# Performance work log

Hardware: AMD Instinct MI355X
Metric: run time of the kernel (lower is better)

The kernel has to match this reference:

```python
import jax, jax.numpy as jnp
import numpy as np

EMBED = 1024
HEADS = 16
HEAD_DIM = EMBED // HEADS


def setup_inputs() -> dict:
    key = jax.random.key(0)
    ks = jax.random.split(key, 6)
    N, L = 2, 2048
    s = 1.0 / np.sqrt(EMBED)
    x = jax.random.normal(ks[0], (N, L, EMBED), dtype=jnp.float32)
    Wq = jax.random.normal(ks[1], (EMBED, EMBED), dtype=jnp.float32) * s
    Wk = jax.random.normal(ks[2], (EMBED, EMBED), dtype=jnp.float32) * s
    Wv = jax.random.normal(ks[3], (EMBED, EMBED), dtype=jnp.float32) * s
    Wo = jax.random.normal(ks[4], (EMBED, EMBED), dtype=jnp.float32) * s
    bo = jax.random.normal(ks[5], (EMBED,), dtype=jnp.float32) * 0.01
    return {"x": x, "Wq": Wq, "Wk": Wk, "Wv": Wv, "Wo": Wo, "bo": bo}


def reference(x, Wq, Wk, Wv, Wo, bo):
    N, L, E = x.shape
    # QKV projections (torch Linear: x @ W.T), split into heads: (N, L, H, D)
    q = (x @ Wq.T).reshape(N, L, HEADS, HEAD_DIM)
    k = (x @ Wk.T).reshape(N, L, HEADS, HEAD_DIM)
    v = (x @ Wv.T).reshape(N, L, HEADS, HEAD_DIM)
    # scores: (N, H, Lq, Lk), scaled by 1/sqrt(embed_size) as in the source
    scores = jnp.einsum("nqhd,nkhd->nhqk", q, k) / jnp.sqrt(jnp.float32(E))
    attn = jax.nn.softmax(scores, axis=-1)
    out = jnp.einsum("nhqk,nkhd->nqhd", attn, v).reshape(N, L, E)
    return out @ Wo.T + bo
```

## Files before the change

### kernel.cpp

```cpp
#include <hip/hip_runtime.h>
#include <hip/hip_bf16.h>
#include <stdint.h>


#define SEQ    2048
#define EMBED  1024
#define QS     3072
#define MTOT   4096
#define SOFTMAX_C 0.04508422002778011f

using bf16x8 = __attribute__((ext_vector_type(8))) __bf16;
using bf16x4 = __attribute__((ext_vector_type(4))) __bf16;
using f32x4  = __attribute__((ext_vector_type(4))) float;

__device__ __forceinline__ unsigned short f2bf(float f) {
  unsigned u = __builtin_bit_cast(unsigned, f);
  u += 0x7fffu + ((u >> 16) & 1u);
  return (unsigned short)(u >> 16);
}
__device__ __forceinline__ float bf2f(unsigned short h) {
  return __builtin_bit_cast(float, (unsigned)h << 16);
}

__device__ __forceinline__ void gl_lds16(const void* g, void* l) {
  __builtin_amdgcn_global_load_lds(
      (const __attribute__((address_space(1))) unsigned int*)g,
      (__attribute__((address_space(3))) unsigned int*)l, 16, 0, 0);
}

__global__ void __launch_bounds__(256) convert_all(
    const float* __restrict__ x, const float* __restrict__ Wq,
    const float* __restrict__ Wk, const float* __restrict__ Wv,
    const float* __restrict__ Wo, unsigned short* __restrict__ xbf,
    unsigned short* __restrict__ wqkv, unsigned short* __restrict__ wo) {
  int b = blockIdx.x;
  int c4 = threadIdx.x << 2;
  const float* src;
  unsigned short* dst;
  if (b < 4096) {
    src = x + (size_t)b * EMBED;
    dst = xbf + (size_t)b * 1024;
  } else if (b < 7168) {
    int R = b - 4096;
    const float* W = (R < 1024) ? Wq : (R < 2048) ? Wk : Wv;
    src = W + (size_t)(R & 1023) * EMBED;
    dst = wqkv + (size_t)R * 1024;
  } else {
    int r = b - 7168;
    src = Wo + (size_t)r * EMBED;
    dst = wo + (size_t)r * 1024;
  }
  float4 v = *(const float4*)(src + c4);
  *(ushort4*)(dst + c4) = make_ushort4(f2bf(v.x), f2bf(v.y), f2bf(v.z), f2bf(v.w));
}

template <int MODE>
__global__ void __launch_bounds__(256, 4) gemm_bt(
    const unsigned short* __restrict__ A, const unsigned short* __restrict__ B,
    void* __restrict__ Cout, const float* __restrict__ bias) {
  constexpr int BM   = (MODE == 0) ? 128 : 64;
  constexpr int LDA  = (MODE == 0) ? 1024 : 2048;
  constexpr int LDB  = 1024;
  constexpr int KTOT = (MODE == 0) ? 1024 : 2048;
  constexpr int NOUT = (MODE == 0) ? 3072 : 1024;
  constexpr int NBX  = NOUT / 128;
  constexpr int NWG  = (MTOT / BM) * NBX;
  constexpr int MI   = BM / 32;
  constexpr int AI   = BM / 32;

  __shared__ __align__(16) unsigned short Alds[BM * 64];
  __shared__ __align__(16) unsigned short Blds[128 * 64];
  const int tid = threadIdx.x;
  const int w = tid >> 6, lane = tid & 63;
  const int g = lane >> 4, l15 = lane & 15;

  int bid = blockIdx.y * NBX + blockIdx.x;
  int swz = (bid & 7) * (NWG / 8) + (bid >> 3);
  const int brow = (swz / NBX) * BM, bcol = (swz % NBX) * 128;
  const int wr = (w >> 1) * (BM / 2), wc = (w & 1) * 64;
  f32x4 acc[MI][4] = {};

  int rsA[AI], csA[AI], rsB[4], csB[4];
#pragma unroll
  for (int i = 0; i < AI; ++i) {
    int L = (i * 4 + w) * 1024 + lane * 16;
    int E = L ^ ((L >> 3) & 0x70);
    rsA[i] = E >> 7;
    csA[i] = (E & 127) >> 1;
  }
#pragma unroll
  for (int i = 0; i < 4; ++i) {
    int L = (i * 4 + w) * 1024 + lane * 16;
    int E = L ^ ((L >> 3) & 0x70);
    rsB[i] = E >> 7;
    csB[i] = (E & 127) >> 1;
  }

  for (int kt = 0; kt < KTOT / 64; ++kt) {
    const int k0 = kt << 6;
    const int k0b = k0 & 1023;
#pragma unroll
    for (int i = 0; i < AI; ++i)
      gl_lds16(A + (size_t)(brow + rsA[i]) * LDA + k0 + csA[i],
               (char*)Alds + (i * 4 + w) * 1024);
#pragma unroll
    for (int i = 0; i < 4; ++i)
      gl_lds16(B + (size_t)(bcol + rsB[i]) * LDB + k0b + csB[i],
               (char*)Blds + (i * 4 + w) * 1024);
    __syncthreads();
#pragma unroll
    for (int ks = 0; ks < 2; ++ks) {
      bf16x8 af[MI], bfr[4];
#pragma unroll
      for (int mi = 0; mi < MI; ++mi) {
        int row = wr + mi * 16 + l15;
        int byt = ((row << 7) + (ks << 6) + (g << 4)) ^ ((row & 7) << 4);
        af[mi] = *(const bf16x8*)((const char*)Alds + byt);
      }
#pragma unroll
      for (int ni = 0; ni < 4; ++ni) {
        int col = wc + ni * 16 + l15;
        int byt = ((col << 7) + (ks << 6) + (g << 4)) ^ ((col & 7) << 4);
        bfr[ni] = *(const bf16x8*)((const char*)Blds + byt);
      }
#pragma unroll
      for (int mi = 0; mi < MI; ++mi)
#pragma unroll
        for (int ni = 0; ni < 4; ++ni)
          acc[mi][ni] = __builtin_amdgcn_mfma_f32_16x16x32_bf16(af[mi], bfr[ni],
                                                                acc[mi][ni], 0, 0, 0);
    }
    __syncthreads();
  }
#pragma unroll
  for (int mi = 0; mi < MI; ++mi)
#pragma unroll
    for (int ni = 0; ni < 4; ++ni)
#pragma unroll
      for (int j = 0; j < 4; ++j) {
        int row = brow + wr + mi * 16 + g * 4 + j;
        int col = bcol + wc + ni * 16 + l15;
        if (MODE == 0) {
          ((unsigned short*)Cout)[(size_t)row * NOUT + col] = f2bf(acc[mi][ni][j]);
        } else {
          ((float*)Cout)[(size_t)row * NOUT + col] = acc[mi][ni][j] + bias[col];
        }
      }
}

__global__ void __launch_bounds__(256, 4) attn_kernel(
    const unsigned short* __restrict__ QKV, float* __restrict__ O0,
    float* __restrict__ O1, float* __restrict__ l0, float* __restrict__ l1) {
  __shared__ __align__(16) unsigned short Klds[64 * 72];
  __shared__ __align__(16) unsigned short Vt[64 * 72];
  __shared__ __align__(16) unsigned short Plds[4][32 * 72];
  const int tid = threadIdx.x, w = tid >> 6, lane = tid & 63;
  const int g = lane >> 4, l15 = lane & 15;
  const int b = blockIdx.x;
  const int swz = (b & 7) * 128 + (b >> 3);
  const int qt = swz & 15, h = (swz >> 4) & 15, n = (swz >> 8) & 1, half = (swz >> 9) & 1;
  const int qbase = qt * 128 + w * 32;
  const size_t rowbase = (size_t)n * SEQ;

  bf16x8 qf[2][2];
#pragma unroll
  for (int mi = 0; mi < 2; ++mi)
#pragma unroll
    for (int ks = 0; ks < 2; ++ks)
      qf[mi][ks] = *(const bf16x8*)(QKV + (rowbase + qbase + mi * 16 + l15) * QS +
                                    h * 64 + ks * 32 + g * 8);
  float lsum[2] = {};
  f32x4 accO[2][4] = {};
  const int kr = tid >> 2, kc = (tid & 3) << 4;
  const int vr = (tid >> 3) << 1, vc = (tid & 7) << 3;
  const int vx = (tid & 7) << 4;

  for (int kt = half * 16; kt < half * 16 + 16; ++kt) {
    {
      const unsigned short* s =
          QKV + (rowbase + kt * 64 + kr) * QS + EMBED + h * 64 + kc;
      uint4 v0 = *(const uint4*)s;
      uint4 v1 = *(const uint4*)(s + 8);
      *(uint4*)&Klds[kr * 72 + kc] = v0;
      *(uint4*)&Klds[kr * 72 + kc + 8] = v1;
    }
    {
      const unsigned short* s =
          QKV + (rowbase + kt * 64 + vr) * QS + 2 * EMBED + h * 64 + vc;
      uint4 a = *(const uint4*)s;
      uint4 bq = *(const uint4*)(s + QS);
      unsigned aw[4] = {a.x, a.y, a.z, a.w};
      unsigned bw[4] = {bq.x, bq.y, bq.z, bq.w};
      char* vb = (char*)Vt;
#pragma unroll
      for (int i = 0; i < 4; ++i) {
        unsigned p0 = (aw[i] & 0xffffu) | (bw[i] << 16);
        unsigned p1 = (aw[i] >> 16) | (bw[i] & 0xffff0000u);
        *(unsigned*)(vb + ((((vc + 2 * i) * 72 + vr) * 2) ^ vx)) = p0;
        *(unsigned*)(vb + ((((vc + 2 * i + 1) * 72 + vr) * 2) ^ vx)) = p1;
      }
    }
    __syncthreads();

    bf16x8 bk[4][2];
#pragma unroll
    for (int ni = 0; ni < 4; ++ni)
#pragma unroll
      for (int ks = 0; ks < 2; ++ks)
        bk[ni][ks] = *(const bf16x8*)&Klds[(ni * 16 + l15) * 72 + ks * 32 + g * 8];
    f32x4 sf[2][4];
    __builtin_amdgcn_s_setprio(1);
#pragma unroll
    for (int mi = 0; mi < 2; ++mi)
#pragma unroll
      for (int ni = 0; ni < 4; ++ni) {
        f32x4 z = {0.f, 0.f, 0.f, 0.f};
        z = __builtin_amdgcn_mfma_f32_16x16x32_bf16(bk[ni][0], qf[mi][0], z, 0, 0, 0);
        sf[mi][ni] =
            __builtin_amdgcn_mfma_f32_16x16x32_bf16(bk[ni][1], qf[mi][1], z, 0, 0, 0);
      }
    __builtin_amdgcn_s_setprio(0);

    unsigned short* Pw = &Plds[w][0];
#pragma unroll
    for (int mi = 0; mi < 2; ++mi)
#pragma unroll
      for (int ni = 0; ni < 4; ++ni) {
        float p0 = __builtin_amdgcn_exp2f(sf[mi][ni][0] * SOFTMAX_C);
        float p1 = __builtin_amdgcn_exp2f(sf[mi][ni][1] * SOFTMAX_C);
        float p2 = __builtin_amdgcn_exp2f(sf[mi][ni][2] * SOFTMAX_C);
        float p3 = __builtin_amdgcn_exp2f(sf[mi][ni][3] * SOFTMAX_C);
        lsum[mi] += (p0 + p1) + (p2 + p3);
        bf16x4 pk = {(__bf16)p0, (__bf16)p1, (__bf16)p2, (__bf16)p3};
        *(bf16x4*)&Pw[(mi * 16 + l15) * 72 + ni * 16 + g * 4] = pk;
      }

    __builtin_amdgcn_s_setprio(1);
#pragma unroll
    for (int ks2 = 0; ks2 < 2; ++ks2) {
      bf16x8 ap0 = *(const bf16x8*)&Pw[l15 * 72 + ks2 * 32 + g * 8];
      bf16x8 ap1 = *(const bf16x8*)&Pw[(16 + l15) * 72 + ks2 * 32 + g * 8];
#pragma unroll
      for (int nd = 0; nd < 4; ++nd) {
        int d = nd * 16 + l15;
        int rb = (d * 144 + (ks2 * 32 + g * 8) * 2) ^ (((d >> 3) & 7) << 4);
        bf16x8 bv = *(const bf16x8*)((const char*)Vt + rb);
        accO[0][nd] = __builtin_amdgcn_mfma_f32_16x16x32_bf16(ap0, bv, accO[0][nd], 0, 0, 0);
        accO[1][nd] = __builtin_amdgcn_mfma_f32_16x16x32_bf16(ap1, bv, accO[1][nd], 0, 0, 0);
      }
    }
    __builtin_amdgcn_s_setprio(0);
    __syncthreads();
  }

  float* Opart = half ? O1 : O0;
  float* lpart = half ? l1 : l0;
#pragma unroll
  for (int mi = 0; mi < 2; ++mi) {
    float l = lsum[mi];
    l += __shfl_xor(l, 16, 64);
    l += __shfl_xor(l, 32, 64);
    if (g == 0)
      lpart[(n * 16 + h) * SEQ + qbase + mi * 16 + l15] = l;
#pragma unroll
    for (int nd = 0; nd < 4; ++nd)
#pragma unroll
      for (int j = 0; j < 4; ++j) {
        int row = qbase + mi * 16 + g * 4 + j;
        Opart[(rowbase + row) * EMBED + h * 64 + nd * 16 + l15] = accO[mi][nd][j];
      }
  }
}

__global__ void __launch_bounds__(256) merge_convert(
    const float* __restrict__ O0, const float* __restrict__ O1,
    const float* __restrict__ l0, const float* __restrict__ l1,
    unsigned short* __restrict__ ocat) {
  int r = blockIdx.x;
  int c4 = threadIdx.x << 2;
  int n = r >> 11, q = r & 2047, h = c4 >> 6;
  float4 a = *(const float4*)(O0 + (size_t)r * EMBED + c4);
  float4 bq = *(const float4*)(O1 + (size_t)r * EMBED + c4);
  int li = (n * 16 + h) * SEQ + q;
  float linv = 1.0f / (l0[li] + l1[li]);
  float vv[4] = {(a.x + bq.x) * linv, (a.y + bq.y) * linv,
                 (a.z + bq.z) * linv, (a.w + bq.w) * linv};
  unsigned short hx[4], lo[4];
#pragma unroll
  for (int i = 0; i < 4; ++i) {
    hx[i] = f2bf(vv[i]);
    lo[i] = f2bf(vv[i] - bf2f(hx[i]));
  }
  unsigned short* d = ocat + (size_t)r * 2048 + c4;
  *(ushort4*)(d)        = make_ushort4(hx[0], hx[1], hx[2], hx[3]);
  *(ushort4*)(d + 1024) = make_ushort4(lo[0], lo[1], lo[2], lo[3]);
}

extern "C" void kernel_launch(void* const* d_in, const int* in_sizes, int n_in,
                              void* d_out, int out_size, void* d_ws, size_t ws_size,
                              hipStream_t stream) {
  const float* x  = (const float*)d_in[0];
  const float* Wq = (const float*)d_in[1];
  const float* Wk = (const float*)d_in[2];
  const float* Wv = (const float*)d_in[3];
  const float* Wo = (const float*)d_in[4];
  const float* bo = (const float*)d_in[5];

  char* ws = (char*)d_ws;
  unsigned short* wo    = (unsigned short*)(ws);
  unsigned short* xbf   = (unsigned short*)(ws + 2097152);
  unsigned short* wqkv  = (unsigned short*)(ws + 10485760);
  unsigned short* qkv   = (unsigned short*)(ws + 16777216);
  float* l0p = (float*)(ws + 2097152);
  float* l1p = (float*)(ws + 2359296);
  float* O0  = (float*)(ws + 41943040);
  float* O1  = (float*)(ws + 58720256);
  unsigned short* ocat = qkv;

  convert_all<<<8192, 256, 0, stream>>>(x, Wq, Wk, Wv, Wo, xbf, wqkv, wo);

  gemm_bt<0><<<dim3(3072 / 128, MTOT / 128), 256, 0, stream>>>(xbf, wqkv, qkv, nullptr);

  attn_kernel<<<1024, 256, 0, stream>>>(qkv, O0, O1, l0p, l1p);
  merge_convert<<<4096, 256, 0, stream>>>(O0, O1, l0p, l1p, ocat);

  gemm_bt<1><<<dim3(1024 / 128, MTOT / 64), 256, 0, stream>>>(ocat, wo, d_out, bo);
}
```

Measured before the change: 199.8 us.

## Use 32x32 MFMA with register-resident P via permlane swap in attention

Attention now computes transposed scores (S^T = K·Q^T) with 32x32x16 MFMAs, so each lane holds one query's probabilities. A permlane32 swap rearranges them into the B operand of the PV MFMA, which removes the per-wave P staging through LDS. K/V global loads for the next tile are prefetched into registers while the current tile is processed. The output is written transposed (d-major), and merge_convert is rewritten to transpose back through an LDS tile. This adds register pressure and moves the strided stores into a separate transpose pass.

```diff
diff --git a/kernel.cpp b/kernel.cpp
--- a/kernel.cpp
+++ b/kernel.cpp
@@ -10,8 +10,10 @@
 #define SOFTMAX_C 0.04508422002778011f
 
 using bf16x8 = __attribute__((ext_vector_type(8))) __bf16;
-using bf16x4 = __attribute__((ext_vector_type(4))) __bf16;
 using f32x4  = __attribute__((ext_vector_type(4))) float;
+using f32x16 = __attribute__((ext_vector_type(16))) float;
+using u32x4  = __attribute__((ext_vector_type(4))) unsigned;
+typedef int v2i __attribute__((ext_vector_type(2)));
 
 __device__ __forceinline__ unsigned short f2bf(float f) {
   unsigned u = __builtin_bit_cast(unsigned, f);
@@ -20,6 +22,24 @@
 }
 __device__ __forceinline__ float bf2f(unsigned short h) {
   return __builtin_bit_cast(float, (unsigned)h << 16);
+}
+__device__ __forceinline__ unsigned pk2(float a, float b) {
+  return (unsigned)f2bf(a) | ((unsigned)f2bf(b) << 16);
+}
+__device__ __forceinline__ void pl32swap(unsigned& a, unsigned& b) {
+#if __has_builtin(__builtin_amdgcn_permlane32_swap)
+  v2i r = __builtin_amdgcn_permlane32_swap((int)a, (int)b, false, false);
+  a = (unsigned)r.x;
+  b = (unsigned)r.y;
+#else
+  unsigned xa = (unsigned)__shfl_xor((int)a, 32, 64);
+  unsigned xb = (unsigned)__shfl_xor((int)b, 32, 64);
+  bool hi = (threadIdx.x & 63) >= 32;
+  unsigned na = hi ? xb : a;
+  unsigned nb = hi ? b : xa;
+  a = na;
+  b = nb;
+#endif
 }
 
 __device__ __forceinline__ void gl_lds16(const void* g, void* l) {
@@ -148,152 +168,177 @@
       }
 }
 
+template <int B0, int SG>
+__device__ __forceinline__ void proc_half(const f32x16& sf, const unsigned short* Vt_,
+                                          int l31, int hi, float& lsum,
+                                          f32x16& accO0, f32x16& accO1) {
+  float e0 = __builtin_amdgcn_exp2f(sf[B0 + 0] * SOFTMAX_C);
+  float e1 = __builtin_amdgcn_exp2f(sf[B0 + 1] * SOFTMAX_C);
+  float e2 = __builtin_amdgcn_exp2f(sf[B0 + 2] * SOFTMAX_C);
+  float e3 = __builtin_amdgcn_exp2f(sf[B0 + 3] * SOFTMAX_C);
+  float e4 = __builtin_amdgcn_exp2f(sf[B0 + 4] * SOFTMAX_C);
+  float e5 = __builtin_amdgcn_exp2f(sf[B0 + 5] * SOFTMAX_C);
+  float e6 = __builtin_amdgcn_exp2f(sf[B0 + 6] * SOFTMAX_C);
+  float e7 = __builtin_amdgcn_exp2f(sf[B0 + 7] * SOFTMAX_C);
+  lsum += ((e0 + e1) + (e2 + e3)) + ((e4 + e5) + (e6 + e7));
+  unsigned w0 = pk2(e0, e1), w1 = pk2(e2, e3), w2 = pk2(e4, e5), w3 = pk2(e6, e7);
+  pl32swap(w0, w2);
+  pl32swap(w1, w3);
+  u32x4 fw = {w0, w1, w2, w3};
+  bf16x8 pf = __builtin_bit_cast(bf16x8, fw);
+  {
+    int d = l31;
+    int byt = (d * 144 + SG * 32 + hi * 16) ^ (((d >> 3) & 7) << 4);
+    bf16x8 vf = *(const bf16x8*)((const char*)Vt_ + byt);
+    accO0 = __builtin_amdgcn_mfma_f32_32x32x16_bf16(vf, pf, accO0, 0, 0, 0);
+  }
+  {
+    int d = 32 + l31;
+    int byt = (d * 144 + SG * 32 + hi * 16) ^ (((d >> 3) & 7) << 4);
+    bf16x8 vf = *(const bf16x8*)((const char*)Vt_ + byt);
+    accO1 = __builtin_amdgcn_mfma_f32_32x32x16_bf16(vf, pf, accO1, 0, 0, 0);
+  }
+}
+
 __global__ void __launch_bounds__(256, 4) attn_kernel(
-    const unsigned short* __restrict__ QKV, float* __restrict__ O0,
-    float* __restrict__ O1, float* __restrict__ l0, float* __restrict__ l1) {
+    const unsigned short* __restrict__ QKV, float* __restrict__ O0T,
+    float* __restrict__ O1T, float* __restrict__ l0, float* __restrict__ l1) {
   __shared__ __align__(16) unsigned short Klds[64 * 72];
   __shared__ __align__(16) unsigned short Vt[64 * 72];
-  __shared__ __align__(16) unsigned short Plds[4][32 * 72];
   const int tid = threadIdx.x, w = tid >> 6, lane = tid & 63;
-  const int g = lane >> 4, l15 = lane & 15;
+  const int l31 = lane & 31, hi = lane >> 5;
   const int b = blockIdx.x;
   const int swz = (b & 7) * 128 + (b >> 3);
   const int qt = swz & 15, h = (swz >> 4) & 15, n = (swz >> 8) & 1, half = (swz >> 9) & 1;
-  const int qbase = qt * 128 + w * 32;
+  const int nh = n * 16 + h;
+  const int qw = qt * 128 + w * 32 + l31;
   const size_t rowbase = (size_t)n * SEQ;
 
-  bf16x8 qf[2][2];
-#pragma unroll
-  for (int mi = 0; mi < 2; ++mi)
-#pragma unroll
-    for (int ks = 0; ks < 2; ++ks)
-      qf[mi][ks] = *(const bf16x8*)(QKV + (rowbase + qbase + mi * 16 + l15) * QS +
-                                    h * 64 + ks * 32 + g * 8);
-  float lsum[2] = {};
-  f32x4 accO[2][4] = {};
+  bf16x8 qf[4];
+#pragma unroll
+  for (int s = 0; s < 4; ++s)
+    qf[s] = *(const bf16x8*)(QKV + (rowbase + qw) * QS + h * 64 + s * 16 + hi * 8);
+
+  float lsum = 0.f;
+  f32x16 accO0 = {}, accO1 = {};
+
   const int kr = tid >> 2, kc = (tid & 3) << 4;
   const int vr = (tid >> 3) << 1, vc = (tid & 7) << 3;
   const int vx = (tid & 7) << 4;
 
-  for (int kt = half * 16; kt < half * 16 + 16; ++kt) {
+  const int kt0 = half * 16;
+  uint4 ka, kb, va, vb;
+  {
+    const unsigned short* s = QKV + (rowbase + kt0 * 64 + kr) * QS + EMBED + h * 64 + kc;
+    ka = *(const uint4*)s;
+    kb = *(const uint4*)(s + 8);
+    const unsigned short* sv = QKV + (rowbase + kt0 * 64 + vr) * QS + 2 * EMBED + h * 64 + vc;
+    va = *(const uint4*)sv;
+    vb = *(const uint4*)(sv + QS);
+  }
+
+  for (int kt = kt0; kt < kt0 + 16; ++kt) {
+    *(uint4*)&Klds[kr * 72 + kc] = ka;
+    *(uint4*)&Klds[kr * 72 + kc + 8] = kb;
     {
-      const unsigned short* s =
-          QKV + (rowbase + kt * 64 + kr) * QS + EMBED + h * 64 + kc;
-      uint4 v0 = *(const uint4*)s;
-      uint4 v1 = *(const uint4*)(s + 8);
-      *(uint4*)&Klds[kr * 72 + kc] = v0;
-      *(uint4*)&Klds[kr * 72 + kc + 8] = v1;
-    }
-    {
-      const unsigned short* s =
-          QKV + (rowbase + kt * 64 + vr) * QS + 2 * EMBED + h * 64 + vc;
-      uint4 a = *(const uint4*)s;
-      uint4 bq = *(const uint4*)(s + QS);
-      unsigned aw[4] = {a.x, a.y, a.z, a.w};
-      unsigned bw[4] = {bq.x, bq.y, bq.z, bq.w};
-      char* vb = (char*)Vt;
+      unsigned aw[4] = {va.x, va.y, va.z, va.w};
+      unsigned bw[4] = {vb.x, vb.y, vb.z, vb.w};
+      char* vbp = (char*)Vt;
 #pragma unroll
       for (int i = 0; i < 4; ++i) {
         unsigned p0 = (aw[i] & 0xffffu) | (bw[i] << 16);
         unsigned p1 = (aw[i] >> 16) | (bw[i] & 0xffff0000u);
-        *(unsigned*)(vb + ((((vc + 2 * i) * 72 + vr) * 2) ^ vx)) = p0;
-        *(unsigned*)(vb + ((((vc + 2 * i + 1) * 72 + vr) * 2) ^ vx)) = p1;
+        *(unsigned*)(vbp + ((((vc + 2 * i) * 72 + vr) * 2) ^ vx)) = p0;
+        *(unsigned*)(vbp + ((((vc + 2 * i + 1) * 72 + vr) * 2) ^ vx)) = p1;
       }
     }
+    if (kt + 1 < kt0 + 16) {
+      const unsigned short* s =
+          QKV + (rowbase + (kt + 1) * 64 + kr) * QS + EMBED + h * 64 + kc;
+      ka = *(const uint4*)s;
+      kb = *(const uint4*)(s + 8);
+      const unsigned short* sv =
+          QKV + (rowbase + (kt + 1) * 64 + vr) * QS + 2 * EMBED + h * 64 + vc;
+      va = *(const uint4*)sv;
+      vb = *(const uint4*)(sv + QS);
+    }
     __syncthreads();
 
-    bf16x8 bk[4][2];
-#pragma unroll
-    for (int ni = 0; ni < 4; ++ni)
-#pragma unroll
-      for (int ks = 0; ks < 2; ++ks)
-        bk[ni][ks] = *(const bf16x8*)&Klds[(ni * 16 + l15) * 72 + ks * 32 + g * 8];
-    f32x4 sf[2][4];
-    __builtin_amdgcn_s_setprio(1);
-#pragma unroll
-    for (int mi = 0; mi < 2; ++mi)
-#pragma unroll
-      for (int ni = 0; ni < 4; ++ni) {
-        f32x4 z = {0.f, 0.f, 0.f, 0.f};
-        z = __builtin_amdgcn_mfma_f32_16x16x32_bf16(bk[ni][0], qf[mi][0], z, 0, 0, 0);
-        sf[mi][ni] =
-            __builtin_amdgcn_mfma_f32_16x16x32_bf16(bk[ni][1], qf[mi][1], z, 0, 0, 0);
-      }
-    __builtin_amdgcn_s_setprio(0);
-
-    unsigned short* Pw = &Plds[w][0];
-#pragma unroll
-    for (int mi = 0; mi < 2; ++mi)
-#pragma unroll
-      for (int ni = 0; ni < 4; ++ni) {
-        float p0 = __builtin_amdgcn_exp2f(sf[mi][ni][0] * SOFTMAX_C);
-        float p1 = __builtin_amdgcn_exp2f(sf[mi][ni][1] * SOFTMAX_C);
-        float p2 = __builtin_amdgcn_exp2f(sf[mi][ni][2] * SOFTMAX_C);
-        float p3 = __builtin_amdgcn_exp2f(sf[mi][ni][3] * SOFTMAX_C);
-        lsum[mi] += (p0 + p1) + (p2 + p3);
-        bf16x4 pk = {(__bf16)p0, (__bf16)p1, (__bf16)p2, (__bf16)p3};
-        *(bf16x4*)&Pw[(mi * 16 + l15) * 72 + ni * 16 + g * 4] = pk;
-      }
-
-    __builtin_amdgcn_s_setprio(1);
-#pragma unroll
-    for (int ks2 = 0; ks2 < 2; ++ks2) {
-      bf16x8 ap0 = *(const bf16x8*)&Pw[l15 * 72 + ks2 * 32 + g * 8];
-      bf16x8 ap1 = *(const bf16x8*)&Pw[(16 + l15) * 72 + ks2 * 32 + g * 8];
-#pragma unroll
-      for (int nd = 0; nd < 4; ++nd) {
-        int d = nd * 16 + l15;
-        int rb = (d * 144 + (ks2 * 32 + g * 8) * 2) ^ (((d >> 3) & 7) << 4);
-        bf16x8 bv = *(const bf16x8*)((const char*)Vt + rb);
-        accO[0][nd] = __builtin_amdgcn_mfma_f32_16x16x32_bf16(ap0, bv, accO[0][nd], 0, 0, 0);
-        accO[1][nd] = __builtin_amdgcn_mfma_f32_16x16x32_bf16(ap1, bv, accO[1][nd], 0, 0, 0);
-      }
-    }
-    __builtin_amdgcn_s_setprio(0);
+    f32x16 s0t = {};
+#pragma unroll
+    for (int s = 0; s < 4; ++s) {
+      bf16x8 kf = *(const bf16x8*)((const char*)Klds + l31 * 144 + s * 32 + hi * 16);
+      s0t = __builtin_amdgcn_mfma_f32_32x32x16_bf16(kf, qf[s], s0t, 0, 0, 0);
+    }
+    proc_half<0, 0>(s0t, Vt, l31, hi, lsum, accO0, accO1);
+    proc_half<8, 1>(s0t, Vt, l31, hi, lsum, accO0, accO1);
+
+    f32x16 s1t = {};
+#pragma unroll
+    for (int s = 0; s < 4; ++s) {
+      bf16x8 kf = *(const bf16x8*)((const char*)Klds + (32 + l31) * 144 + s * 32 + hi * 16);
+      s1t = __builtin_amdgcn_mfma_f32_32x32x16_bf16(kf, qf[s], s1t, 0, 0, 0);
+    }
+    proc_half<0, 2>(s1t, Vt, l31, hi, lsum, accO0, accO1);
+    proc_half<8, 3>(s1t, Vt, l31, hi, lsum, accO0, accO1);
+
     __syncthreads();
   }
 
-  float* Opart = half ? O1 : O0;
-  float* lpart = half ? l1 : l0;
-#pragma unroll
-  for (int mi = 0; mi < 2; ++mi) {
-    float l = lsum[mi];
-    l += __shfl_xor(l, 16, 64);
-    l += __shfl_xor(l, 32, 64);
-    if (g == 0)
-      lpart[(n * 16 + h) * SEQ + qbase + mi * 16 + l15] = l;
-#pragma unroll
-    for (int nd = 0; nd < 4; ++nd)
-#pragma unroll
-      for (int j = 0; j < 4; ++j) {
-        int row = qbase + mi * 16 + g * 4 + j;
-        Opart[(rowbase + row) * EMBED + h * 64 + nd * 16 + l15] = accO[mi][nd][j];
-      }
+  lsum += __shfl_xor(lsum, 32, 64);
+  float* OT = half ? O1T : O0T;
+  float* lp = half ? l1 : l0;
+  if (hi == 0) lp[nh * SEQ + qw] = lsum;
+  const size_t obase = (size_t)nh * 64 * SEQ + qw;
+#pragma unroll
+  for (int r = 0; r < 16; ++r) {
+    int d0 = (r & 3) + 8 * (r >> 2) + 4 * hi;
+    OT[obase + (size_t)d0 * SEQ] = accO0[r];
+    OT[obase + (size_t)(d0 + 32) * SEQ] = accO1[r];
   }
 }
 
 __global__ void __launch_bounds__(256) merge_convert(
-    const float* __restrict__ O0, const float* __restrict__ O1,
+    const float* __restrict__ O0T, const float* __restrict__ O1T,
     const float* __restrict__ l0, const float* __restrict__ l1,
     unsigned short* __restrict__ ocat) {
-  int r = blockIdx.x;
-  int c4 = threadIdx.x << 2;
-  int n = r >> 11, q = r & 2047, h = c4 >> 6;
-  float4 a = *(const float4*)(O0 + (size_t)r * EMBED + c4);
-  float4 bq = *(const float4*)(O1 + (size_t)r * EMBED + c4);
-  int li = (n * 16 + h) * SEQ + q;
-  float linv = 1.0f / (l0[li] + l1[li]);
-  float vv[4] = {(a.x + bq.x) * linv, (a.y + bq.y) * linv,
-                 (a.z + bq.z) * linv, (a.w + bq.w) * linv};
-  unsigned short hx[4], lo[4];
-#pragma unroll
-  for (int i = 0; i < 4; ++i) {
-    hx[i] = f2bf(vv[i]);
-    lo[i] = f2bf(vv[i] - bf2f(hx[i]));
-  }
-  unsigned short* d = ocat + (size_t)r * 2048 + c4;
-  *(ushort4*)(d)        = make_ushort4(hx[0], hx[1], hx[2], hx[3]);
-  *(ushort4*)(d + 1024) = make_ushort4(lo[0], lo[1], lo[2], lo[3]);
+  __shared__ float ftile[64][132];
+  __shared__ float llds[128];
+  const int b = blockIdx.x;
+  const int nh = b >> 4, qb = b & 15;
+  const int t = threadIdx.x;
+  if (t < 128) {
+    int q = qb * 128 + t;
+    llds[t] = 1.0f / (l0[nh * SEQ + q] + l1[nh * SEQ + q]);
+  }
+  const size_t base = (size_t)nh * 64 * SEQ + qb * 128;
+#pragma unroll
+  for (int p = 0; p < 8; ++p) {
+    int d = (t >> 5) + p * 8;
+    int qq = (t & 31) * 4;
+    float4 a = *(const float4*)(O0T + base + (size_t)d * SEQ + qq);
+    float4 c = *(const float4*)(O1T + base + (size_t)d * SEQ + qq);
+    float4 s4 = {a.x + c.x, a.y + c.y, a.z + c.z, a.w + c.w};
+    *(float4*)&ftile[d][qq] = s4;
+  }
+  __syncthreads();
+  const int q = t >> 1, sect = t & 1;
+  const float linv = llds[q];
+  const int n = nh >> 4, h = nh & 15;
+  unsigned short* orow =
+      ocat + (size_t)(n * SEQ + qb * 128 + q) * 2048 + h * 64 + sect * 32;
+#pragma unroll
+  for (int i = 0; i < 32; i += 4) {
+    unsigned short hx[4], lx[4];
+#pragma unroll
+    for (int k = 0; k < 4; ++k) {
+      float v = ftile[sect * 32 + i + k][q] * linv;
+      hx[k] = f2bf(v);
+      lx[k] = f2bf(v - bf2f(hx[k]));
+    }
+    *(ushort4*)(orow + i) = make_ushort4(hx[0], hx[1], hx[2], hx[3]);
+    *(ushort4*)(orow + 1024 + i) = make_ushort4(lx[0], lx[1], lx[2], lx[3]);
+  }
 }
 
 extern "C" void kernel_launch(void* const* d_in, const int* in_sizes, int n_in,
@@ -313,16 +358,16 @@
   unsigned short* qkv   = (unsigned short*)(ws + 16777216);
   float* l0p = (float*)(ws + 2097152);
   float* l1p = (float*)(ws + 2359296);
-  float* O0  = (float*)(ws + 41943040);
-  float* O1  = (float*)(ws + 58720256);
+  float* O0T = (float*)(ws + 41943040);
+  float* O1T = (float*)(ws + 58720256);
   unsigned short* ocat = qkv;
 
   convert_all<<<8192, 256, 0, stream>>>(x, Wq, Wk, Wv, Wo, xbf, wqkv, wo);
 
   gemm_bt<0><<<dim3(3072 / 128, MTOT / 128), 256, 0, stream>>>(xbf, wqkv, qkv, nullptr);
 
-  attn_kernel<<<1024, 256, 0, stream>>>(qkv, O0, O1, l0p, l1p);
-  merge_convert<<<4096, 256, 0, stream>>>(O0, O1, l0p, l1p, ocat);
+  attn_kernel<<<1024, 256, 0, stream>>>(qkv, O0T, O1T, l0p, l1p);
+  merge_convert<<<512, 256, 0, stream>>>(O0T, O1T, l0p, l1p, ocat);
 
   gemm_bt<1><<<dim3(1024 / 128, MTOT / 64), 256, 0, stream>>>(ocat, wo, d_out, bo);
 }
```

Result: slower. 215.3 us (+7.8%).
